# Kernel optimization log

Hardware: AMD Instinct MI355X
Metric: run time of the kernel (lower is better)

## Reference

```python
import jax, jax.numpy as jnp
import numpy as np

B, N, E, H = 8, 512, 64, 128


def setup_inputs() -> dict:
    key = jax.random.key(0)
    ks = jax.random.split(key, 9)
    s_in = 1.0 / np.sqrt(2 * E)
    s_h = 1.0 / np.sqrt(H)
    s_e = 1.0 / np.sqrt(E)
    return {
        "X": jax.random.normal(ks[0], (B, N, E), dtype=jnp.float32),
        # cross-sim MLP: Linear(2E,H) -> ReLU -> Linear(H,1) -> Sigmoid
        "Wc1": jax.random.uniform(ks[1], (2 * E, H), jnp.float32, -s_in, s_in),
        "bc1": jax.random.uniform(ks[2], (H,), jnp.float32, -s_in, s_in),
        "Wc2": jax.random.uniform(ks[3], (H, 1), jnp.float32, -s_h, s_h),
        "bc2": jax.random.uniform(ks[4], (1,), jnp.float32, -s_h, s_h),
        # self-sim MLP: Linear(E,H) -> ReLU -> Linear(H,1) -> Sigmoid
        "Ws1": jax.random.uniform(ks[5], (E, H), jnp.float32, -s_e, s_e),
        "bs1": jax.random.uniform(ks[6], (H,), jnp.float32, -s_e, s_e),
        "Ws2": jax.random.uniform(ks[7], (H, 1), jnp.float32, -s_h, s_h),
        "bs2": jax.random.uniform(ks[8], (1,), jnp.float32, -s_h, s_h),
    }


def reference(X, Wc1, bc1, Wc2, bc2, Ws1, bs1, Ws2, bs2):
    b, n, _ = X.shape
    idx_i, idx_j = jnp.triu_indices(n, k=1)  # [P], P = n(n-1)/2

    # gather pairwise features: [B, P, 2E]
    X_i = X[:, idx_i, :]
    X_j = X[:, idx_j, :]
    pair = jnp.concatenate([X_i, X_j], axis=-1)

    # tiny cross-sim MLP -> [B, P]
    h = jax.nn.relu(jnp.einsum("bpe,eh->bph", pair, Wc1) + bc1)
    sim_upper = jax.nn.sigmoid(jnp.einsum("bph,ho->bpo", h, Wc2) + bc2)[..., 0]

    # self-sim MLP on the diagonal -> [B, N]
    hd = jax.nn.relu(jnp.einsum("bne,eh->bnh", X, Ws1) + bs1)
    sim_diag = jax.nn.sigmoid(jnp.einsum("bnh,ho->bno", hd, Ws2) + bs2)[..., 0]

    # scatter into symmetric sim matrix [B, N, N]
    sim = jnp.zeros((b, n, n), dtype=X.dtype)
    sim = sim.at[:, idx_i, idx_j].set(sim_upper)
    sim = sim.at[:, idx_j, idx_i].set(sim_upper)
    diag = jnp.arange(n)
    sim = sim.at[:, diag, diag].set(sim_diag)
    return sim
```

## Files before the change

kernel.cpp:

```cpp
#include <hip/hip_runtime.h>

typedef float v4f __attribute__((ext_vector_type(4)));

#define NTOK 512
#define EDIM 64
#define HDIM 128
#define NN   (NTOK*NTOK)

__device__ __forceinline__ float sigf(float x) {
    return __builtin_amdgcn_rcpf(1.f + __expf(-x));
}

__global__ __launch_bounds__(128) void precomp_kernel(
    const float* __restrict__ X, const float* __restrict__ Wc1, const float* __restrict__ bc1,
    const float* __restrict__ Ws1, const float* __restrict__ bs1,
    const float* __restrict__ Ws2, const float* __restrict__ bs2,
    float* __restrict__ Ag, float* __restrict__ Bg, float* __restrict__ out)
{
    __shared__ float Xs[8*EDIM];
    __shared__ float red[8*132];
    const int t  = threadIdx.x;
    const int g0 = blockIdx.x * 8;

    for (int i = t; i < 8*EDIM; i += 128) Xs[i] = X[g0*EDIM + i];
    __syncthreads();

    float accA[8] = {0}, accB[8] = {0}, accS[8] = {0};
    #pragma unroll 8
    for (int e = 0; e < EDIM; e++) {
        float wt = Wc1[e*HDIM + t];
        float wb = Wc1[(EDIM+e)*HDIM + t];
        float ws = Ws1[e*HDIM + t];
        #pragma unroll
        for (int r = 0; r < 8; r++) {
            float x = Xs[r*EDIM + e];
            accA[r] = fmaf(x, wt, accA[r]);
            accB[r] = fmaf(x, wb, accB[r]);
            accS[r] = fmaf(x, ws, accS[r]);
        }
    }
    const float b1 = bc1[t], s1 = bs1[t], w2 = Ws2[t];
    #pragma unroll
    for (int r = 0; r < 8; r++) {
        Ag[(g0+r)*HDIM + t] = accA[r];
        Bg[(g0+r)*HDIM + t] = accB[r] + b1;
        float hd = fmaxf(accS[r] + s1, 0.f);
        red[r*132 + t] = hd * w2;
    }
    __syncthreads();
    if (t < 8) {
        const float* rr = red + t*132;
        float s = 0.f;
        #pragma unroll
        for (int i = 0; i < HDIM/4; i++) {
            v4f v = *(const v4f*)(rr + 4*i);
            s += v[0] + v[1] + v[2] + v[3];
        }
        float val = sigf(s + bs2[0]);
        int g = g0 + t;
        int b = g >> 9, n = g & 511;
        out[b*NN + n*NTOK + n] = val;
    }
}

__global__ __launch_bounds__(256) void pair_kernel(
    const float* __restrict__ Ag, const float* __restrict__ Bg,
    const float* __restrict__ Wc2, const float* __restrict__ bc2,
    float* __restrict__ out)
{
    __shared__ float RowT[64*HDIM];
    __shared__ float ColT[64*HDIM];

    const int t  = threadIdx.x;
    const int tc = blockIdx.x, tr = blockIdx.y, b = blockIdx.z;
    const int r0 = tr*64, c0 = tc*64;

    const float* Rsrc;
    const float* Csrc;
    if (tr <= tc) { Rsrc = Ag + (b*NTOK + r0)*HDIM; Csrc = Bg + (b*NTOK + c0)*HDIM; }
    else          { Rsrc = Bg + (b*NTOK + r0)*HDIM; Csrc = Ag + (b*NTOK + c0)*HDIM; }

    {
        const int hv = t & 31;
        for (int k = t >> 5; k < 64; k += 8) {
            const int sw = 4*(hv ^ (k & 31));
            *(v4f*)(RowT + k*HDIM + sw) = *(const v4f*)(Rsrc + k*HDIM + 4*hv);
            *(v4f*)(ColT + k*HDIM + sw) = *(const v4f*)(Csrc + k*HDIM + 4*hv);
        }
    }
    __syncthreads();

    const int ti = t & 15, tj = t >> 4;
    int rbase[4], rmask[4], cbase[4], cmask[4];
    #pragma unroll
    for (int u = 0; u < 4; u++) {
        int k = ti + 16*u; rbase[u] = k*HDIM; rmask[u] = k & 31;
        int c = 4*tj + u;  cbase[u] = c*HDIM; cmask[u] = c & 31;
    }

    v4f acc[4] = {{0,0,0,0},{0,0,0,0},{0,0,0,0},{0,0,0,0}};
    for (int hq = 0; hq < HDIM/4; hq++) {
        const v4f w4 = *(const v4f*)(Wc2 + 4*hq);
        v4f ra[4], cb[4];
        #pragma unroll
        for (int u = 0; u < 4; u++) ra[u] = *(const v4f*)(RowT + rbase[u] + 4*(hq ^ rmask[u]));
        #pragma unroll
        for (int v = 0; v < 4; v++) cb[v] = *(const v4f*)(ColT + cbase[v] + 4*(hq ^ cmask[v]));
        #pragma unroll
        for (int hh = 0; hh < 4; hh++) {
            #pragma unroll
            for (int u = 0; u < 4; u++) {
                #pragma unroll
                for (int v = 0; v < 4; v++) {
                    float s = fmaxf(ra[u][hh] + cb[v][hh], 0.f);
                    acc[u][v] = fmaf(s, w4[hh], acc[u][v]);
                }
            }
        }
    }

    const float bb   = bc2[0];
    const int obase  = b*NN;
    if (tr == tc) {
        #pragma unroll
        for (int u = 0; u < 4; u++) {
            const int r = r0 + ti + 16*u;
            #pragma unroll
            for (int v = 0; v < 4; v++) {
                const int c = c0 + 4*tj + v;
                if (r < c) {
                    float s = sigf(acc[u][v] + bb);
                    out[obase + r*NTOK + c] = s;
                    out[obase + c*NTOK + r] = s;
                }
            }
        }
    } else {
        #pragma unroll
        for (int u = 0; u < 4; u++) {
            const int r = r0 + ti + 16*u;
            v4f sv;
            #pragma unroll
            for (int v = 0; v < 4; v++) sv[v] = sigf(acc[u][v] + bb);
            *(v4f*)(out + obase + r*NTOK + c0 + 4*tj) = sv;
        }
    }
}

extern "C" void kernel_launch(void* const* d_in, const int* in_sizes, int n_in,
                              void* d_out, int out_size, void* d_ws, size_t ws_size,
                              hipStream_t stream) {
    const float* X   = (const float*)d_in[0];
    const float* Wc1 = (const float*)d_in[1];
    const float* bc1 = (const float*)d_in[2];
    const float* Wc2 = (const float*)d_in[3];
    const float* bc2 = (const float*)d_in[4];
    const float* Ws1 = (const float*)d_in[5];
    const float* bs1 = (const float*)d_in[6];
    const float* Ws2 = (const float*)d_in[7];
    const float* bs2 = (const float*)d_in[8];
    float* out = (float*)d_out;

    float* Ag = (float*)d_ws;
    float* Bg = Ag + 8*NTOK*HDIM;

    precomp_kernel<<<dim3(4096/8), dim3(128), 0, stream>>>(X, Wc1, bc1, Ws1, bs1, Ws2, bs2, Ag, Bg, out);
    pair_kernel<<<dim3(8, 8, 8), dim3(256), 0, stream>>>(Ag, Bg, Wc2, bc2, out);
}
```

Before: 108.8 us.

## Compute only upper-triangle pair tiles and write the mirrored tile via shared transpose

The pair kernel now launches only upper-triangle 64x32 half-tiles (56 off-diagonal plus 16 diagonal halves per batch) instead of all 64 full tiles. Each off-diagonal block writes its tile directly and then transposes it through shared memory to write the symmetric lower tile with coalesced vector stores. This roughly halves the relu-FMA work of the pair MLP, which is the dominant cost. In exchange it adds extra syncs, a shared transpose and a smaller per-thread tile (4x2), which lowers register reuse per LDS load. Wc2 is also staged into shared memory.

```diff
diff --git a/kernel.cpp b/kernel.cpp
--- a/kernel.cpp
+++ b/kernel.cpp
@@ -1,6 +1,7 @@
 #include <hip/hip_runtime.h>
 
 typedef float v4f __attribute__((ext_vector_type(4)));
+typedef float v2f __attribute__((ext_vector_type(2)));
 
 #define NTOK 512
 #define EDIM 64
@@ -69,80 +70,112 @@
     float* __restrict__ out)
 {
     __shared__ float RowT[64*HDIM];
-    __shared__ float ColT[64*HDIM];
-
-    const int t  = threadIdx.x;
-    const int tc = blockIdx.x, tr = blockIdx.y, b = blockIdx.z;
-    const int r0 = tr*64, c0 = tc*64;
-
-    const float* Rsrc;
-    const float* Csrc;
-    if (tr <= tc) { Rsrc = Ag + (b*NTOK + r0)*HDIM; Csrc = Bg + (b*NTOK + c0)*HDIM; }
-    else          { Rsrc = Bg + (b*NTOK + r0)*HDIM; Csrc = Ag + (b*NTOK + c0)*HDIM; }
-
+    __shared__ float ColT[32*HDIM];
+    __shared__ float WcS[HDIM];
+
+    const int t = threadIdx.x;
+    const int b = blockIdx.y;
+    const int u = blockIdx.x;
+    int tr, tc, half;
+    if (u < 56) {
+        int p = u >> 1; half = u & 1;
+        tr = 0; int rem = p;
+        while (rem >= 7 - tr) { rem -= 7 - tr; tr++; }
+        tc = tr + 1 + rem;
+    } else {
+        int d = (u - 56) >> 1; half = u & 1; tr = d; tc = d;
+    }
+    const int r0 = tr*64, c0 = tc*64 + half*32;
+    const bool isdiag = (tr == tc);
+
+    const float* Rsrc = Ag + (b*NTOK + r0)*HDIM;
+    const float* Csrc = Bg + (b*NTOK + c0)*HDIM;
+
+    if (t < 32) *(v4f*)(WcS + 4*t) = *(const v4f*)(Wc2 + 4*t);
     {
         const int hv = t & 31;
         for (int k = t >> 5; k < 64; k += 8) {
             const int sw = 4*(hv ^ (k & 31));
             *(v4f*)(RowT + k*HDIM + sw) = *(const v4f*)(Rsrc + k*HDIM + 4*hv);
+        }
+        for (int k = t >> 5; k < 32; k += 8) {
+            const int sw = 4*(hv ^ k);
             *(v4f*)(ColT + k*HDIM + sw) = *(const v4f*)(Csrc + k*HDIM + 4*hv);
         }
     }
     __syncthreads();
 
-    const int ti = t & 15, tj = t >> 4;
-    int rbase[4], rmask[4], cbase[4], cmask[4];
-    #pragma unroll
-    for (int u = 0; u < 4; u++) {
-        int k = ti + 16*u; rbase[u] = k*HDIM; rmask[u] = k & 31;
-        int c = 4*tj + u;  cbase[u] = c*HDIM; cmask[u] = c & 31;
-    }
-
-    v4f acc[4] = {{0,0,0,0},{0,0,0,0},{0,0,0,0},{0,0,0,0}};
+    const int tj = t & 15, ti = t >> 4;
+    int rbase[4], rmask[4];
+    #pragma unroll
+    for (int uu = 0; uu < 4; uu++) { int k = ti + 16*uu; rbase[uu] = k*HDIM; rmask[uu] = k & 31; }
+    int cbase[2], cmask[2];
+    #pragma unroll
+    for (int v = 0; v < 2; v++) { int c = 2*tj + v; cbase[v] = c*HDIM; cmask[v] = c & 31; }
+
+    float acc[4][2] = {};
     for (int hq = 0; hq < HDIM/4; hq++) {
-        const v4f w4 = *(const v4f*)(Wc2 + 4*hq);
-        v4f ra[4], cb[4];
-        #pragma unroll
-        for (int u = 0; u < 4; u++) ra[u] = *(const v4f*)(RowT + rbase[u] + 4*(hq ^ rmask[u]));
-        #pragma unroll
-        for (int v = 0; v < 4; v++) cb[v] = *(const v4f*)(ColT + cbase[v] + 4*(hq ^ cmask[v]));
+        const v4f w4 = *(const v4f*)(WcS + 4*hq);
+        v4f ra[4], cb[2];
+        #pragma unroll
+        for (int uu = 0; uu < 4; uu++) ra[uu] = *(const v4f*)(RowT + rbase[uu] + 4*(hq ^ rmask[uu]));
+        #pragma unroll
+        for (int v = 0; v < 2; v++)   cb[v]  = *(const v4f*)(ColT + cbase[v] + 4*(hq ^ cmask[v]));
         #pragma unroll
         for (int hh = 0; hh < 4; hh++) {
             #pragma unroll
-            for (int u = 0; u < 4; u++) {
+            for (int uu = 0; uu < 4; uu++) {
                 #pragma unroll
-                for (int v = 0; v < 4; v++) {
-                    float s = fmaxf(ra[u][hh] + cb[v][hh], 0.f);
-                    acc[u][v] = fmaf(s, w4[hh], acc[u][v]);
+                for (int v = 0; v < 2; v++) {
+                    float s = fmaxf(ra[uu][hh] + cb[v][hh], 0.f);
+                    acc[uu][v] = fmaf(s, w4[hh], acc[uu][v]);
                 }
             }
         }
     }
 
-    const float bb   = bc2[0];
-    const int obase  = b*NN;
-    if (tr == tc) {
-        #pragma unroll
-        for (int u = 0; u < 4; u++) {
-            const int r = r0 + ti + 16*u;
+    const float bb = bc2[0];
+    float* outb = out + b*NN;
+    float sv[4][2];
+    #pragma unroll
+    for (int uu = 0; uu < 4; uu++)
+        #pragma unroll
+        for (int v = 0; v < 2; v++) sv[uu][v] = sigf(acc[uu][v] + bb);
+
+    if (!isdiag) {
+        #pragma unroll
+        for (int uu = 0; uu < 4; uu++) {
+            int r = r0 + ti + 16*uu;
+            v2f p; p[0] = sv[uu][0]; p[1] = sv[uu][1];
+            *(v2f*)(outb + r*NTOK + c0 + 2*tj) = p;
+        }
+        __syncthreads();
+        float* Tb = ColT;
+        #pragma unroll
+        for (int uu = 0; uu < 4; uu++)
             #pragma unroll
-            for (int v = 0; v < 4; v++) {
-                const int c = c0 + 4*tj + v;
+            for (int v = 0; v < 2; v++)
+                Tb[(2*tj + v)*68 + ti + 16*uu] = sv[uu][v];
+        __syncthreads();
+        const int q = t >> 3, x0 = (t & 7) * 8;
+        const float* src = Tb + q*68 + x0;
+        v4f a0 = *(const v4f*)src;
+        v4f a1 = *(const v4f*)(src + 4);
+        float* drow = outb + (c0 + q)*NTOK + r0 + x0;
+        *(v4f*)drow = a0;
+        *(v4f*)(drow + 4) = a1;
+    } else {
+        #pragma unroll
+        for (int uu = 0; uu < 4; uu++) {
+            int r = r0 + ti + 16*uu;
+            #pragma unroll
+            for (int v = 0; v < 2; v++) {
+                int c = c0 + 2*tj + v;
                 if (r < c) {
-                    float s = sigf(acc[u][v] + bb);
-                    out[obase + r*NTOK + c] = s;
-                    out[obase + c*NTOK + r] = s;
+                    outb[r*NTOK + c] = sv[uu][v];
+                    outb[c*NTOK + r] = sv[uu][v];
                 }
             }
-        }
-    } else {
-        #pragma unroll
-        for (int u = 0; u < 4; u++) {
-            const int r = r0 + ti + 16*u;
-            v4f sv;
-            #pragma unroll
-            for (int v = 0; v < 4; v++) sv[v] = sigf(acc[u][v] + bb);
-            *(v4f*)(out + obase + r*NTOK + c0 + 4*tj) = sv;
         }
     }
 }
@@ -165,5 +198,5 @@
     float* Bg = Ag + 8*NTOK*HDIM;
 
     precomp_kernel<<<dim3(4096/8), dim3(128), 0, stream>>>(X, Wc1, bc1, Ws1, bs1, Ws2, bs2, Ag, Bg, out);
-    pair_kernel<<<dim3(8, 8, 8), dim3(256), 0, stream>>>(Ag, Bg, Wc2, bc2, out);
-}
+    pair_kernel<<<dim3(72, 8), dim3(256), 0, stream>>>(Ag, Bg, Wc2, bc2, out);
+}
```

Result: faster. 104.5 us (-4.0%).
